# Performance work log

Hardware: AMD Instinct MI355X
Metric: run time of the kernel (lower is better)

## Reference

```python
import jax, jax.numpy as jnp
import numpy as np


def setup_inputs() -> dict:
    key = jax.random.key(0)
    kq, kk, kv = jax.random.split(key, 3)
    B, H, S, D = 4, 16, 2048, 64
    q = jax.random.normal(kq, (B, H, S, D), dtype=jnp.float32)
    k = jax.random.normal(kk, (B, H, S, D), dtype=jnp.float32)
    v = jax.random.normal(kv, (B, H, S, D), dtype=jnp.float32)
    # causal mask: True = attend, broadcasts over batch/head dims
    mask = jnp.tril(jnp.ones((S, S), dtype=bool))
    return {"q": q, "k": k, "v": v, "mask": mask}


def reference(q, k, v, mask):
    # att[b,h,i,j] = q[b,h,i,:] . k[b,h,j,:] / sqrt(d_k)
    scale = 1.0 / jnp.sqrt(jnp.asarray(k.shape[-1], dtype=q.dtype))
    att = jnp.einsum('bhqd,bhkd->bhqk', q, k) * scale
    att = jnp.where(mask, att, -jnp.inf)  # additive -inf mask, equivalent to att + where(mask,0,-inf)
    att = jax.nn.softmax(att, axis=-1)
    return jnp.einsum('bhqk,bhkd->bhqd', att, v)
```

## Files before the change

### kernel.cpp

```cpp
#include <hip/hip_runtime.h>
#include <hip/hip_bf16.h>

typedef __attribute__((ext_vector_type(4)))  float f32x4;
typedef __attribute__((ext_vector_type(16))) float f32x16;
typedef __attribute__((ext_vector_type(8)))  short bf16x8;
typedef __attribute__((ext_vector_type(4)))  short bf16x4;

constexpr int SEQ = 2048;
constexpr int DH  = 64;
constexpr int BH  = 64;
constexpr int QB  = 128;
constexpr int KB  = 64;
constexpr int NQT = SEQ / QB;
constexpr int NST = SEQ / 64;

__device__ __forceinline__ short f2bf(float f) {
    union { float f; unsigned u; } x; x.f = f;
    unsigned r = x.u + 0x7fffu + ((x.u >> 16) & 1u);
    return (short)(r >> 16);
}

__device__ __forceinline__ unsigned cvtpk(float lo, float hi) {
    unsigned r;
    asm("v_cvt_pk_bf16_f32 %0, %1, %2" : "=v"(r) : "v"(lo), "v"(hi));
    return r;
}

__device__ __forceinline__ float exp2fast(float x) {
#if __has_builtin(__builtin_amdgcn_exp2f)
    return __builtin_amdgcn_exp2f(x);
#else
    float r;
    asm("v_exp_f32 %0, %1\n\ts_nop 0" : "=v"(r) : "v"(x));
    return r;
#endif
}

__device__ __forceinline__ void half_swap(unsigned a, unsigned b, unsigned &x, unsigned &y) {
#if __has_builtin(__builtin_amdgcn_permlane32_swap)
    auto rr = __builtin_amdgcn_permlane32_swap(a, b, false, false);
    x = rr[0]; y = rr[1];
#else
    unsigned as = (unsigned)__shfl_xor((int)a, 32);
    unsigned bs = (unsigned)__shfl_xor((int)b, 32);
    const bool lo = ((threadIdx.x & 63) < 32);
    x = lo ? a : bs;
    y = lo ? as : b;
#endif
}

__global__ __launch_bounds__(256) void prep_kernel(
    const float* __restrict__ Kg, const float* __restrict__ Vg,
    short* __restrict__ Kb, short* __restrict__ Vt)
{
    __shared__ short sT[64][66];
    const int bid = blockIdx.x;
    const int bh  = bid & (BH - 1);
    const int st  = bid >> 6;
    const int s0  = st * 64;
    const size_t base = (size_t)bh * SEQ * DH;
    const int tid = threadIdx.x;

    #pragma unroll
    for (int it = 0; it < 4; ++it) {
        const int i4 = it * 256 + tid;
        const int r  = i4 >> 4;
        const int c4 = (i4 & 15) << 2;
        const size_t gidx = base + (size_t)(s0 + r) * DH + c4;
        f32x4 kx = *(const f32x4*)(Kg + gidx);
        bf16x4 kb4;
        #pragma unroll
        for (int j = 0; j < 4; ++j) kb4[j] = f2bf(kx[j]);
        *(bf16x4*)(Kb + gidx) = kb4;
        f32x4 vx = *(const f32x4*)(Vg + gidx);
        #pragma unroll
        for (int j = 0; j < 4; ++j) sT[r][c4 + j] = f2bf(vx[j]);
    }
    __syncthreads();

    const int d   = tid >> 2;
    const int seg = (tid & 3) * 16;
    bf16x8 lo, hi;
    #pragma unroll
    for (int m = 0; m < 8; ++m) { lo[m] = sT[seg + m][d]; hi[m] = sT[seg + 8 + m][d]; }
    short* Vo = Vt + base + (size_t)d * SEQ + (s0 + seg);
    *(bf16x8*)Vo       = lo;
    *(bf16x8*)(Vo + 8) = hi;
}

__global__ __launch_bounds__(256, 4) void fattn7_kernel(
    const float* __restrict__ Qg, const short* __restrict__ Kb,
    const short* __restrict__ Vt, float* __restrict__ Og)
{
    __shared__ short sK[2][KB * DH];
    __shared__ short sV[2][DH * KB];

    const int bid  = blockIdx.x;
    const int xcd  = bid & 7;
    const int pass = bid >> 8;
    const int slot = (bid >> 3) & 31;
    const int bh   = xcd * 8 + (slot >> 2);
    const int a    = slot & 3;
    const int qt   = (pass == 0) ? (15 - a) : (pass == 1) ? (8 + a)
                   : (pass == 2) ? (7 - a)  : a;
    const int q0   = qt * QB;

    const int tid  = threadIdx.x;
    const int wid  = tid >> 6;
    const int lane = tid & 63;
    const int l31  = lane & 31;
    const int hi   = lane >> 5;

    const size_t base = (size_t)bh * SEQ * DH;
    const float* Qb = Qg + base;
    const short* Kp = Kb + base;
    const short* Vp = Vt + base;

    const int qw = q0 + wid * 32;
    const int qr = qw + l31;

    const int rrow = wid * 16 + (lane >> 3);
    const int cs   = (lane & 7) ^ (rrow & 7);
    const short* kSrc = Kp + (size_t)rrow * DH + cs * 8;
    const short* vSrc = Vp + (size_t)rrow * SEQ + cs * 8;

    auto ISSUE = [&](int t, int buf) {
        const int kv0 = t * KB;
        __builtin_amdgcn_global_load_lds((const unsigned int*)(kSrc + (size_t)kv0 * DH),
                                         (unsigned int*)&sK[buf][wid * 1024], 16, 0, 0);
        __builtin_amdgcn_global_load_lds((const unsigned int*)(kSrc + (size_t)kv0 * DH + 8 * DH),
                                         (unsigned int*)&sK[buf][wid * 1024 + 512], 16, 0, 0);
        __builtin_amdgcn_global_load_lds((const unsigned int*)(vSrc + kv0),
                                         (unsigned int*)&sV[buf][wid * 1024], 16, 0, 0);
        __builtin_amdgcn_global_load_lds((const unsigned int*)(vSrc + kv0 + 8 * SEQ),
                                         (unsigned int*)&sV[buf][wid * 1024 + 512], 16, 0, 0);
    };

    ISSUE(0, 0);

    constexpr float QSCALE = 0.125f * 1.44269504088896340736f;
    bf16x8 qf[4];
    #pragma unroll
    for (int dt = 0; dt < 4; ++dt) {
        const float* qp = Qb + (size_t)qr * DH + dt * 16 + hi * 8;
        f32x4 av = *(const f32x4*)qp;
        f32x4 bv = *(const f32x4*)(qp + 4);
        bf16x8 f;
        #pragma unroll
        for (int j = 0; j < 4; ++j) { f[j] = f2bf(av[j] * QSCALE); f[j + 4] = f2bf(bv[j] * QSCALE); }
        qf[dt] = f;
    }

    f32x16 z16;
    #pragma unroll
    for (int r = 0; r < 16; ++r) z16[r] = 0.f;

    f32x16 o0, o1;
    #pragma unroll
    for (int r = 0; r < 16; ++r) { o0[r] = 0.f; o1[r] = 0.f; }
    float m_i = -1e30f, l_i = 0.f;

    const int ntile = 2 * qt + 2;
    __syncthreads();

    for (int t = 0; t < ntile; ++t) {
        const int kv0 = t * KB;
        const int cur = t & 1;
        if (t + 1 < ntile) ISSUE(t + 1, cur ^ 1);

        if (kv0 <= qw + 31) {
            const short* cK = &sK[cur][0];
            const short* cV = &sV[cur][0];

            f32x16 st0, st1;
            __builtin_amdgcn_s_setprio(1);
            {
                const int ca0 = hi * 16;
                bf16x8 k0 = *(const bf16x8*)((const char*)cK + l31 * 128 + (ca0 ^ ((l31 & 7) << 4)));
                bf16x8 k1 = *(const bf16x8*)((const char*)cK + (32 + l31) * 128 + (ca0 ^ ((l31 & 7) << 4)));
                st0 = __builtin_amdgcn_mfma_f32_32x32x16_bf16(k0, qf[0], z16, 0, 0, 0);
                st1 = __builtin_amdgcn_mfma_f32_32x32x16_bf16(k1, qf[0], z16, 0, 0, 0);
            }
            #pragma unroll
            for (int dt = 1; dt < 4; ++dt) {
                const int ca = dt * 32 + hi * 16;
                bf16x8 k0 = *(const bf16x8*)((const char*)cK + l31 * 128 + (ca ^ ((l31 & 7) << 4)));
                bf16x8 k1 = *(const bf16x8*)((const char*)cK + (32 + l31) * 128 + (ca ^ ((l31 & 7) << 4)));
                st0 = __builtin_amdgcn_mfma_f32_32x32x16_bf16(k0, qf[dt], st0, 0, 0, 0);
                st1 = __builtin_amdgcn_mfma_f32_32x32x16_bf16(k1, qf[dt], st1, 0, 0, 0);
            }
            __builtin_amdgcn_s_setprio(0);

            if (kv0 + KB - 1 > qw) {
                #pragma unroll
                for (int r = 0; r < 16; ++r) {
                    const int kr = (r & 3) + 8 * (r >> 2) + 4 * hi;
                    if (kv0 + kr > qr)      st0[r] = -1e30f;
                    if (kv0 + 32 + kr > qr) st1[r] = -1e30f;
                }
            }

            float mx[8];
            #pragma unroll
            for (int r = 0; r < 8; ++r)
                mx[r] = fmaxf(fmaxf(st0[r], st0[r + 8]), fmaxf(st1[r], st1[r + 8]));
            #pragma unroll
            for (int s = 4; s > 0; s >>= 1)
                #pragma unroll
                for (int r = 0; r < s; ++r) mx[r] = fmaxf(mx[r], mx[r + s]);
            float pm = fmaxf(mx[0], __shfl_xor(mx[0], 32));

            constexpr float THR = 8.0f * 1.44269504088896340736f;
            if (!__all(pm - m_i <= THR)) {
                const float nm = fmaxf(m_i, pm);
                const float cf = exp2fast(m_i - nm);
                #pragma unroll
                for (int r = 0; r < 16; ++r) {
                    const int kr = (r & 3) + 8 * (r >> 2) + 4 * hi;
                    const float cfr = __shfl(cf, kr);
                    o0[r] *= cfr; o1[r] *= cfr;
                }
                l_i *= cf;
                m_i = nm;
            }

            float rs0 = 0.f, rs1 = 0.f, rs2 = 0.f, rs3 = 0.f;
            #pragma unroll
            for (int r = 0; r < 16; r += 4) {
                st0[r]     = exp2fast(st0[r]     - m_i); rs0 += st0[r];
                st0[r + 1] = exp2fast(st0[r + 1] - m_i); rs1 += st0[r + 1];
                st0[r + 2] = exp2fast(st0[r + 2] - m_i); rs2 += st0[r + 2];
                st0[r + 3] = exp2fast(st0[r + 3] - m_i); rs3 += st0[r + 3];
            }
            #pragma unroll
            for (int r = 0; r < 16; r += 4) {
                st1[r]     = exp2fast(st1[r]     - m_i); rs0 += st1[r];
                st1[r + 1] = exp2fast(st1[r + 1] - m_i); rs1 += st1[r + 1];
                st1[r + 2] = exp2fast(st1[r + 2] - m_i); rs2 += st1[r + 2];
                st1[r + 3] = exp2fast(st1[r + 3] - m_i); rs3 += st1[r + 3];
            }
            float rs = (rs0 + rs1) + (rs2 + rs3);
            rs += __shfl_xor(rs, 32);
            l_i += rs;

            bf16x8 pf[4];
            {
                unsigned pk[8];
                #pragma unroll
                for (int i = 0; i < 8; ++i) pk[i] = cvtpk(st0[2 * i], st0[2 * i + 1]);
                #pragma unroll
                for (int cc = 0; cc < 2; ++cc) {
                    unsigned x0, y0, x1, y1;
                    half_swap(pk[4 * cc + 0], pk[4 * cc + 2], x0, y0);
                    half_swap(pk[4 * cc + 1], pk[4 * cc + 3], x1, y1);
                    union { unsigned u[4]; bf16x8 v; } uu;
                    uu.u[0] = x0; uu.u[1] = x1; uu.u[2] = y0; uu.u[3] = y1;
                    pf[cc] = uu.v;
                }
                #pragma unroll
                for (int i = 0; i < 8; ++i) pk[i] = cvtpk(st1[2 * i], st1[2 * i + 1]);
                #pragma unroll
                for (int cc = 0; cc < 2; ++cc) {
                    unsigned x0, y0, x1, y1;
                    half_swap(pk[4 * cc + 0], pk[4 * cc + 2], x0, y0);
                    half_swap(pk[4 * cc + 1], pk[4 * cc + 3], x1, y1);
                    union { unsigned u[4]; bf16x8 v; } uu;
                    uu.u[0] = x0; uu.u[1] = x1; uu.u[2] = y0; uu.u[3] = y1;
                    pf[2 + cc] = uu.v;
                }
            }

            __builtin_amdgcn_s_setprio(1);
            #pragma unroll
            for (int ks = 0; ks < 4; ++ks) {
                const int cv = ks * 32 + hi * 16;
                bf16x8 v0 = *(const bf16x8*)((const char*)cV + l31 * 128 + (cv ^ ((l31 & 7) << 4)));
                o0 = __builtin_amdgcn_mfma_f32_32x32x16_bf16(pf[ks], v0, o0, 0, 0, 0);
                bf16x8 v1 = *(const bf16x8*)((const char*)cV + (32 + l31) * 128 + (cv ^ ((l31 & 7) << 4)));
                o1 = __builtin_amdgcn_mfma_f32_32x32x16_bf16(pf[ks], v1, o1, 0, 0, 0);
            }
            __builtin_amdgcn_s_setprio(0);
        }

        __syncthreads();
    }

    float* Ob = Og + base;
    #pragma unroll
    for (int r = 0; r < 16; ++r) {
        const int kr  = (r & 3) + 8 * (r >> 2) + 4 * hi;
        const float ll = __shfl(l_i, kr);
        const float inv = 1.0f / ll;
        const int row = qw + kr;
        Ob[(size_t)row * DH + l31]      = o0[r] * inv;
        Ob[(size_t)row * DH + 32 + l31] = o1[r] * inv;
    }
}

extern "C" void kernel_launch(void* const* d_in, const int* in_sizes, int n_in,
                              void* d_out, int out_size, void* d_ws, size_t ws_size,
                              hipStream_t stream) {
    const float* q = (const float*)d_in[0];
    const float* k = (const float*)d_in[1];
    const float* v = (const float*)d_in[2];
    float* out = (float*)d_out;

    short* Kb = (short*)d_ws;
    short* Vt = Kb + (size_t)BH * SEQ * DH;

    prep_kernel<<<dim3(BH * NST), dim3(256), 0, stream>>>(k, v, Kb, Vt);
    fattn7_kernel<<<dim3(BH * NQT), dim3(256), 0, stream>>>(q, Kb, Vt, out);
}
```

Before: 77.43 us.

## Software-pipeline PV of previous tile with QK of current tile

Restructures the KV loop so the P·V MFMAs for tile t-1 run in the same iteration as the Q·K MFMAs for tile t. This lets matrix work overlap the softmax exp and max latency instead of serialising them. V gets a third LDS buffer so the previous tile's V stays live while the next one is prefetched, and a tail handles the final PV. The cross-half max reduction also switches to permlane32_swap. The cost is more LDS per block, which could reduce occupancy, and more live registers for the carried P fragments.

```diff
diff --git a/kernel.cpp b/kernel.cpp
--- a/kernel.cpp
+++ b/kernel.cpp
@@ -46,6 +46,18 @@
     const bool lo = ((threadIdx.x & 63) < 32);
     x = lo ? a : bs;
     y = lo ? as : b;
+#endif
+}
+
+__device__ __forceinline__ float maxhalf(float v) {
+#if __has_builtin(__builtin_amdgcn_permlane32_swap)
+    union { float f; unsigned u; } a; a.f = v;
+    auto rr = __builtin_amdgcn_permlane32_swap(a.u, a.u, false, false);
+    union { unsigned u; float f; } x, y;
+    x.u = rr[0]; y.u = rr[1];
+    return fmaxf(x.f, y.f);
+#else
+    return fmaxf(v, __shfl_xor(v, 32));
 #endif
 }
 
@@ -88,12 +100,12 @@
     *(bf16x8*)(Vo + 8) = hi;
 }
 
-__global__ __launch_bounds__(256, 4) void fattn7_kernel(
+__global__ __launch_bounds__(256, 4) void fattn9_kernel(
     const float* __restrict__ Qg, const short* __restrict__ Kb,
     const short* __restrict__ Vt, float* __restrict__ Og)
 {
     __shared__ short sK[2][KB * DH];
-    __shared__ short sV[2][DH * KB];
+    __shared__ short sV[3][DH * KB];
 
     const int bid  = blockIdx.x;
     const int xcd  = bid & 7;
@@ -116,27 +128,28 @@
     const short* Kp = Kb + base;
     const short* Vp = Vt + base;
 
-    const int qw = q0 + wid * 32;
-    const int qr = qw + l31;
+    const int qw    = q0 + wid * 32;
+    const int qr    = qw + l31;
+    const int lastT = (qw + 31) >> 6;
 
     const int rrow = wid * 16 + (lane >> 3);
     const int cs   = (lane & 7) ^ (rrow & 7);
     const short* kSrc = Kp + (size_t)rrow * DH + cs * 8;
     const short* vSrc = Vp + (size_t)rrow * SEQ + cs * 8;
 
-    auto ISSUE = [&](int t, int buf) {
-        const int kv0 = t * KB;
+    auto ISSUE = [&](int t1, int kb, int vs) {
+        const int kv0 = t1 * KB;
         __builtin_amdgcn_global_load_lds((const unsigned int*)(kSrc + (size_t)kv0 * DH),
-                                         (unsigned int*)&sK[buf][wid * 1024], 16, 0, 0);
+                                         (unsigned int*)&sK[kb][wid * 1024], 16, 0, 0);
         __builtin_amdgcn_global_load_lds((const unsigned int*)(kSrc + (size_t)kv0 * DH + 8 * DH),
-                                         (unsigned int*)&sK[buf][wid * 1024 + 512], 16, 0, 0);
+                                         (unsigned int*)&sK[kb][wid * 1024 + 512], 16, 0, 0);
         __builtin_amdgcn_global_load_lds((const unsigned int*)(vSrc + kv0),
-                                         (unsigned int*)&sV[buf][wid * 1024], 16, 0, 0);
+                                         (unsigned int*)&sV[vs][wid * 1024], 16, 0, 0);
         __builtin_amdgcn_global_load_lds((const unsigned int*)(vSrc + kv0 + 8 * SEQ),
-                                         (unsigned int*)&sV[buf][wid * 1024 + 512], 16, 0, 0);
+                                         (unsigned int*)&sV[vs][wid * 1024 + 512], 16, 0, 0);
     };
 
-    ISSUE(0, 0);
+    ISSUE(0, 0, 0);
 
     constexpr float QSCALE = 0.125f * 1.44269504088896340736f;
     bf16x8 qf[4];
@@ -159,20 +172,23 @@
     #pragma unroll
     for (int r = 0; r < 16; ++r) { o0[r] = 0.f; o1[r] = 0.f; }
     float m_i = -1e30f, l_i = 0.f;
+    bf16x8 pf0, pf1, pf2, pf3;
 
     const int ntile = 2 * qt + 2;
     __syncthreads();
 
+    int vIss = 1;
+    int vPV  = 2;
+
     for (int t = 0; t < ntile; ++t) {
-        const int kv0 = t * KB;
-        const int cur = t & 1;
-        if (t + 1 < ntile) ISSUE(t + 1, cur ^ 1);
-
-        if (kv0 <= qw + 31) {
-            const short* cK = &sK[cur][0];
-            const short* cV = &sV[cur][0];
-
-            f32x16 st0, st1;
+        if (t + 1 < ntile) ISSUE(t + 1, (t + 1) & 1, vIss);
+
+        const bool doQK = (t <= lastT);
+        const bool doPV = (t >= 1) & (t <= lastT + 1);
+
+        f32x16 st0, st1;
+        if (doQK) {
+            const short* cK = &sK[t & 1][0];
             __builtin_amdgcn_s_setprio(1);
             {
                 const int ca0 = hi * 16;
@@ -190,7 +206,44 @@
                 st1 = __builtin_amdgcn_mfma_f32_32x32x16_bf16(k1, qf[dt], st1, 0, 0, 0);
             }
             __builtin_amdgcn_s_setprio(0);
-
+        }
+
+        if (doPV) {
+            const short* cV = &sV[vPV][0];
+            __builtin_amdgcn_s_setprio(1);
+            {
+                const int cv0 = hi * 16;
+                bf16x8 v0 = *(const bf16x8*)((const char*)cV + l31 * 128 + (cv0 ^ ((l31 & 7) << 4)));
+                bf16x8 v1 = *(const bf16x8*)((const char*)cV + (32 + l31) * 128 + (cv0 ^ ((l31 & 7) << 4)));
+                o0 = __builtin_amdgcn_mfma_f32_32x32x16_bf16(pf0, v0, o0, 0, 0, 0);
+                o1 = __builtin_amdgcn_mfma_f32_32x32x16_bf16(pf0, v1, o1, 0, 0, 0);
+            }
+            {
+                const int cv1 = 32 + hi * 16;
+                bf16x8 v0 = *(const bf16x8*)((const char*)cV + l31 * 128 + (cv1 ^ ((l31 & 7) << 4)));
+                bf16x8 v1 = *(const bf16x8*)((const char*)cV + (32 + l31) * 128 + (cv1 ^ ((l31 & 7) << 4)));
+                o0 = __builtin_amdgcn_mfma_f32_32x32x16_bf16(pf1, v0, o0, 0, 0, 0);
+                o1 = __builtin_amdgcn_mfma_f32_32x32x16_bf16(pf1, v1, o1, 0, 0, 0);
+            }
+            {
+                const int cv2 = 64 + hi * 16;
+                bf16x8 v0 = *(const bf16x8*)((const char*)cV + l31 * 128 + (cv2 ^ ((l31 & 7) << 4)));
+                bf16x8 v1 = *(const bf16x8*)((const char*)cV + (32 + l31) * 128 + (cv2 ^ ((l31 & 7) << 4)));
+                o0 = __builtin_amdgcn_mfma_f32_32x32x16_bf16(pf2, v0, o0, 0, 0, 0);
+                o1 = __builtin_amdgcn_mfma_f32_32x32x16_bf16(pf2, v1, o1, 0, 0, 0);
+            }
+            {
+                const int cv3 = 96 + hi * 16;
+                bf16x8 v0 = *(const bf16x8*)((const char*)cV + l31 * 128 + (cv3 ^ ((l31 & 7) << 4)));
+                bf16x8 v1 = *(const bf16x8*)((const char*)cV + (32 + l31) * 128 + (cv3 ^ ((l31 & 7) << 4)));
+                o0 = __builtin_amdgcn_mfma_f32_32x32x16_bf16(pf3, v0, o0, 0, 0, 0);
+                o1 = __builtin_amdgcn_mfma_f32_32x32x16_bf16(pf3, v1, o1, 0, 0, 0);
+            }
+            __builtin_amdgcn_s_setprio(0);
+        }
+
+        if (doQK) {
+            const int kv0 = t * KB;
             if (kv0 + KB - 1 > qw) {
                 #pragma unroll
                 for (int r = 0; r < 16; ++r) {
@@ -208,7 +261,7 @@
             for (int s = 4; s > 0; s >>= 1)
                 #pragma unroll
                 for (int r = 0; r < s; ++r) mx[r] = fmaxf(mx[r], mx[r + s]);
-            float pm = fmaxf(mx[0], __shfl_xor(mx[0], 32));
+            const float pm = maxhalf(mx[0]);
 
             constexpr float THR = 8.0f * 1.44269504088896340736f;
             if (!__all(pm - m_i <= THR)) {
@@ -243,46 +296,40 @@
             rs += __shfl_xor(rs, 32);
             l_i += rs;
 
-            bf16x8 pf[4];
             {
                 unsigned pk[8];
                 #pragma unroll
                 for (int i = 0; i < 8; ++i) pk[i] = cvtpk(st0[2 * i], st0[2 * i + 1]);
-                #pragma unroll
-                for (int cc = 0; cc < 2; ++cc) {
-                    unsigned x0, y0, x1, y1;
-                    half_swap(pk[4 * cc + 0], pk[4 * cc + 2], x0, y0);
-                    half_swap(pk[4 * cc + 1], pk[4 * cc + 3], x1, y1);
-                    union { unsigned u[4]; bf16x8 v; } uu;
-                    uu.u[0] = x0; uu.u[1] = x1; uu.u[2] = y0; uu.u[3] = y1;
-                    pf[cc] = uu.v;
-                }
+                unsigned x0, y0, x1, y1;
+                half_swap(pk[0], pk[2], x0, y0); half_swap(pk[1], pk[3], x1, y1);
+                { union { unsigned u[4]; bf16x8 v; } uu; uu.u[0]=x0; uu.u[1]=x1; uu.u[2]=y0; uu.u[3]=y1; pf0 = uu.v; }
+                half_swap(pk[4], pk[6], x0, y0); half_swap(pk[5], pk[7], x1, y1);
+                { union { unsigned u[4]; bf16x8 v; } uu; uu.u[0]=x0; uu.u[1]=x1; uu.u[2]=y0; uu.u[3]=y1; pf1 = uu.v; }
                 #pragma unroll
                 for (int i = 0; i < 8; ++i) pk[i] = cvtpk(st1[2 * i], st1[2 * i + 1]);
-                #pragma unroll
-                for (int cc = 0; cc < 2; ++cc) {
-                    unsigned x0, y0, x1, y1;
-                    half_swap(pk[4 * cc + 0], pk[4 * cc + 2], x0, y0);
-                    half_swap(pk[4 * cc + 1], pk[4 * cc + 3], x1, y1);
-                    union { unsigned u[4]; bf16x8 v; } uu;
-                    uu.u[0] = x0; uu.u[1] = x1; uu.u[2] = y0; uu.u[3] = y1;
-                    pf[2 + cc] = uu.v;
-                }
-            }
-
-            __builtin_amdgcn_s_setprio(1);
-            #pragma unroll
-            for (int ks = 0; ks < 4; ++ks) {
-                const int cv = ks * 32 + hi * 16;
-                bf16x8 v0 = *(const bf16x8*)((const char*)cV + l31 * 128 + (cv ^ ((l31 & 7) << 4)));
-                o0 = __builtin_amdgcn_mfma_f32_32x32x16_bf16(pf[ks], v0, o0, 0, 0, 0);
-                bf16x8 v1 = *(const bf16x8*)((const char*)cV + (32 + l31) * 128 + (cv ^ ((l31 & 7) << 4)));
-                o1 = __builtin_amdgcn_mfma_f32_32x32x16_bf16(pf[ks], v1, o1, 0, 0, 0);
-            }
-            __builtin_amdgcn_s_setprio(0);
+                half_swap(pk[0], pk[2], x0, y0); half_swap(pk[1], pk[3], x1, y1);
+                { union { unsigned u[4]; bf16x8 v; } uu; uu.u[0]=x0; uu.u[1]=x1; uu.u[2]=y0; uu.u[3]=y1; pf2 = uu.v; }
+                half_swap(pk[4], pk[6], x0, y0); half_swap(pk[5], pk[7], x1, y1);
+                { union { unsigned u[4]; bf16x8 v; } uu; uu.u[0]=x0; uu.u[1]=x1; uu.u[2]=y0; uu.u[3]=y1; pf3 = uu.v; }
+            }
         }
 
         __syncthreads();
+        vIss = (vIss == 2) ? 0 : vIss + 1;
+        vPV  = (vPV == 2) ? 0 : vPV + 1;
+    }
+
+    if (lastT == ntile - 1) {
+        const short* cV = &sV[vPV][0];
+        #pragma unroll
+        for (int ks = 0; ks < 4; ++ks) {
+            const int cv = ks * 32 + hi * 16;
+            bf16x8 v0 = *(const bf16x8*)((const char*)cV + l31 * 128 + (cv ^ ((l31 & 7) << 4)));
+            bf16x8 v1 = *(const bf16x8*)((const char*)cV + (32 + l31) * 128 + (cv ^ ((l31 & 7) << 4)));
+            const bf16x8 pfk = (ks == 0) ? pf0 : (ks == 1) ? pf1 : (ks == 2) ? pf2 : pf3;
+            o0 = __builtin_amdgcn_mfma_f32_32x32x16_bf16(pfk, v0, o0, 0, 0, 0);
+            o1 = __builtin_amdgcn_mfma_f32_32x32x16_bf16(pfk, v1, o1, 0, 0, 0);
+        }
     }
 
     float* Ob = Og + base;
@@ -309,5 +356,5 @@
     short* Vt = Kb + (size_t)BH * SEQ * DH;
 
     prep_kernel<<<dim3(BH * NST), dim3(256), 0, stream>>>(k, v, Kb, Vt);
-    fattn7_kernel<<<dim3(BH * NQT), dim3(256), 0, stream>>>(q, Kb, Vt, out);
-}
+    fattn9_kernel<<<dim3(BH * NQT), dim3(256), 0, stream>>>(q, Kb, Vt, out);
+}
```

Result: slower. 113.7 us (+46.9%).
